# Kernel optimization log

Measured on AMD Instinct MI355X. Metric: run time of the kernel, lower is better.

## Reference

```python
import jax, jax.numpy as jnp
import numpy as np

B, S, D, H = 1, 2048, 768, 12
E, K, I = 8, 2, 1024          # routed experts, top-k, expert inter dim
IS = 2 * I                    # shared-expert inter dim (n_shared_experts * moe_inter_dim)
EPS = 1e-5
ROUTE_SCALE = 1.0


def rmsnorm(x, w, eps=EPS):
    xf = x.astype(jnp.float32)
    return (xf * jax.lax.rsqrt(jnp.mean(xf * xf, axis=-1, keepdims=True) + eps)).astype(x.dtype) * w


def setup_inputs() -> dict:
    key = jax.random.key(0)
    ks = jax.random.split(key, 8)
    sc = 0.02
    return {
        "x": jax.random.normal(ks[0], (B, S, D), jnp.float32),
        "norm1_w": jnp.ones((D,), jnp.float32),
        "norm3_w": jnp.ones((D,), jnp.float32),
        "gate_w": jax.random.normal(ks[1], (E, D), jnp.float32) * sc,
        "w1": jax.random.normal(ks[2], (E, I, D), jnp.float32) * sc,
        "b1": jnp.zeros((E, I), jnp.float32),
        "w2": jax.random.normal(ks[3], (E, D, I), jnp.float32) * sc,
        "b2": jnp.zeros((E, D), jnp.float32),
        "w3": jax.random.normal(ks[4], (E, I, D), jnp.float32) * sc,
        "b3": jnp.zeros((E, I), jnp.float32),
        "fc1_w": jax.random.normal(ks[5], (IS, D), jnp.float32) * sc,
        "fc1_b": jnp.zeros((IS,), jnp.float32),
        "fc2_w": jax.random.normal(ks[6], (D, IS), jnp.float32) * sc,
        "fc2_b": jnp.zeros((D,), jnp.float32),
    }


def _forward(x, norm1_w, norm3_w, gate_w, w1, b1, w2, b2, w3, b3,
             fc1_w, fc1_b, fc2_w, fc2_b):
    b, s, d = x.shape
    hd = d // H

    # ---- self-attention (no qkv/out projections in the original module) ----
    xn = rmsnorm(x, norm1_w)
    qkv = xn.reshape(b, s, H, hd).transpose(0, 2, 1, 3)      # [b,h,s,hd]
    scores = jnp.einsum("bhqd,bhkd->bhqk", qkv, qkv) / np.sqrt(hd)
    attn = jax.nn.softmax(scores, axis=-1)
    ao = jnp.einsum("bhqk,bhkd->bhqd", attn, qkv)
    attn_out = ao.transpose(0, 2, 1, 3).reshape(b, s, d)
    out = x + attn_out

    # ---- MoE on norm3(out) ----
    xf = rmsnorm(out, norm3_w).reshape(-1, d)                # [N, D]
    n = xf.shape[0]

    # Gate: softmax scoring, n_groups=1 (no group masking), no bias (dim != 7168)
    logits = xf @ gate_w.T                                    # [N, E]
    sc = jax.nn.softmax(logits.astype(jnp.float32), axis=-1)  # max-subtract folded in
    _, idx = jax.lax.top_k(sc, K)                             # [N, K]
    weights = jnp.take_along_axis(sc, idx, axis=-1)
    weights = jnp.clip(weights, 1e-7) * ROUTE_SCALE
    weights = weights.astype(xf.dtype)

    # combine matrix: per-token dense expert weights (zeros for unselected)
    cmb = jnp.zeros((n, E), xf.dtype).at[jnp.arange(n)[:, None], idx].add(weights)

    # SwiGLU experts, batched over E (zero combine weight == not dispatched)
    a = jnp.einsum("nd,eid->nei", xf, w1) + b1                # [N,E,I]
    g = jnp.einsum("nd,eid->nei", xf, w3) + b3
    h = jax.nn.silu(a) * g
    eo = jnp.einsum("nei,edi->ned", h, w2) + b2               # [N,E,D]
    y = jnp.einsum("ned,ne->nd", eo, cmb)

    # shared experts (SiLU MLP)
    z = jax.nn.silu(xf @ fc1_w.T + fc1_b) @ fc2_w.T + fc2_b

    moe_out = (y + z).reshape(b, s, d)
    return out + moe_out


def reference(x, norm1_w, norm3_w, gate_w, w1, b1, w2, b2, w3, b3,
              fc1_w, fc1_b, fc2_w, fc2_b):
    return _forward(x, norm1_w, norm3_w, gate_w, w1, b1, w2, b2, w3, b3,
                    fc1_w, fc1_b, fc2_w, fc2_b)
```

## Files before the change

### kernel.cpp

```cpp
#include <hip/hip_runtime.h>
#include <math.h>

#define SEQ    2048
#define DMODEL 768
#define NHEAD  12
#define NEXP   8
#define IDIM   1024
#define ISH    2048
#define KVS    4
#define NE2    10

typedef unsigned short u16;
typedef short s16x8 __attribute__((ext_vector_type(8)));
typedef u16   u16x8 __attribute__((ext_vector_type(8)));
typedef float f32x4 __attribute__((ext_vector_type(4)));

#define MFMA_BF16(a, b, c) __builtin_amdgcn_mfma_f32_16x16x32_bf16((a), (b), (c), 0, 0, 0)

__device__ __forceinline__ void glds16(const void* g, void* l) {
  __builtin_amdgcn_global_load_lds(
      (const __attribute__((address_space(1))) unsigned int*)g,
      (__attribute__((address_space(3))) unsigned int*)l, 16, 0, 0);
}

__device__ __forceinline__ u16 f2b(float f) {
  unsigned int u = __float_as_uint(f);
  unsigned int r = u + 0x7fffu + ((u >> 16) & 1u);
  return (u16)(r >> 16);
}
__device__ __forceinline__ float b2f(u16 v) {
  return __uint_as_float(((unsigned int)v) << 16);
}

__global__ __launch_bounds__(256) void cvt_all_kernel(
    const float* __restrict__ w1, const float* __restrict__ w3, const float* __restrict__ w2,
    const float* __restrict__ fc1, const float* __restrict__ fc2,
    u16* __restrict__ w1b, u16* __restrict__ w3b, u16* __restrict__ w2b,
    u16* __restrict__ fc1b, u16* __restrict__ fc2b, int* __restrict__ counts) {
  if (blockIdx.x == 0 && threadIdx.x < 16) counts[threadIdx.x] = 0;
  long i = (long)blockIdx.x * 256 + threadIdx.x;
  const long NW8 = (long)NEXP * IDIM * DMODEL / 8;
  const long NF8 = (long)ISH * DMODEL / 8;
  const float* s; u16* d; long o;
  if      (i < NW8)             { s = w1;  d = w1b;  o = i; }
  else if (i < 2 * NW8)         { s = w3;  d = w3b;  o = i - NW8; }
  else if (i < 3 * NW8)         { s = w2;  d = w2b;  o = i - 2 * NW8; }
  else if (i < 3 * NW8 + NF8)   { s = fc1; d = fc1b; o = i - 3 * NW8; }
  else if (i < 3 * NW8 + 2*NF8) { s = fc2; d = fc2b; o = i - 3 * NW8 - NF8; }
  else return;
  float4 a = ((const float4*)s)[2 * o], b = ((const float4*)s)[2 * o + 1];
  u16x8 v;
  v[0] = f2b(a.x); v[1] = f2b(a.y); v[2] = f2b(a.z); v[3] = f2b(a.w);
  v[4] = f2b(b.x); v[5] = f2b(b.y); v[6] = f2b(b.z); v[7] = f2b(b.w);
  ((u16x8*)d)[o] = v;
}

__global__ __launch_bounds__(256) void rmsnorm_kernel(const float* __restrict__ in,
                                                      const float* __restrict__ w,
                                                      u16* __restrict__ outb) {
  int row = blockIdx.x;
  int tid = threadIdx.x;
  const float* r = in + (size_t)row * DMODEL;
  float v0 = r[tid], v1 = r[tid + 256], v2 = r[tid + 512];
  float ss = v0 * v0 + v1 * v1 + v2 * v2;
  __shared__ float red[256];
  red[tid] = ss;
  __syncthreads();
  for (int s = 128; s > 0; s >>= 1) {
    if (tid < s) red[tid] += red[tid + s];
    __syncthreads();
  }
  float rms = rsqrtf(red[0] * (1.f / DMODEL) + 1e-5f);
  u16* ob = outb + (size_t)row * DMODEL;
  ob[tid]       = f2b(v0 * rms * w[tid]);
  ob[tid + 256] = f2b(v1 * rms * w[tid + 256]);
  ob[tid + 512] = f2b(v2 * rms * w[tid + 512]);
}

__global__ __launch_bounds__(256) void attn_kernel(const u16* __restrict__ xnb,
                                                   u16* __restrict__ Opart,
                                                   float* __restrict__ Mpart,
                                                   float* __restrict__ Lpart) {
  __shared__ u16 Qs[64][72];
  __shared__ u16 Ks[64][72];
  __shared__ u16 Vt[64][72];
  __shared__ u16 Ps[64][72];
  const int h = blockIdx.y, kvs = blockIdx.z;
  const int q0 = blockIdx.x * 64;
  const int tid = threadIdx.x;
  const int lane = tid & 63, w = tid >> 6;
  const int quad = lane >> 4, l15 = lane & 15;
  const size_t hoff = (size_t)h * 64;

  for (int cc = tid; cc < 512; cc += 256) {
    int row = cc >> 3, col8 = (cc & 7) * 8;
    *(u16x8*)&Qs[row][col8] = *(const u16x8*)(xnb + (size_t)(q0 + row) * DMODEL + hoff + col8);
  }
  __syncthreads();
  const s16x8 aq0 = *(const s16x8*)&Qs[16 * w + l15][quad * 8];
  const s16x8 aq1 = *(const s16x8*)&Qs[16 * w + l15][32 + quad * 8];

  f32x4 o[4] = {};
  float mrow[4], lrow[4];
#pragma unroll
  for (int r = 0; r < 4; r++) { mrow[r] = -INFINITY; lrow[r] = 0.f; }

  const int it0 = kvs * (SEQ / 64 / KVS);
  for (int it = 0; it < SEQ / 64 / KVS; it++) {
    const int k0 = (it0 + it) * 64;
    for (int cc = tid; cc < 512; cc += 256) {
      int row = cc >> 3, col8 = (cc & 7) * 8;
      *(u16x8*)&Ks[row][col8] = *(const u16x8*)(xnb + (size_t)(k0 + row) * DMODEL + hoff + col8);
    }
    __syncthreads();

    {
      const int rp = tid & 31, dc = ((tid >> 5) & 7) * 8;
      u16x8 v0 = *(const u16x8*)&Ks[2 * rp][dc];
      u16x8 v1 = *(const u16x8*)&Ks[2 * rp + 1][dc];
#pragma unroll
      for (int j = 0; j < 8; j++) {
        *(unsigned int*)&Vt[dc + j][2 * rp] =
            (unsigned int)v0[j] | ((unsigned int)v1[j] << 16);
      }
    }

    f32x4 s4[4] = {};
#pragma unroll
    for (int jt = 0; jt < 4; jt++) {
      s16x8 b0 = *(const s16x8*)&Ks[16 * jt + l15][quad * 8];
      s16x8 b1 = *(const s16x8*)&Ks[16 * jt + l15][32 + quad * 8];
      s4[jt] = MFMA_BF16(aq0, b0, s4[jt]);
      s4[jt] = MFMA_BF16(aq1, b1, s4[jt]);
      s4[jt] *= 0.125f;
    }

#pragma unroll
    for (int r = 0; r < 4; r++) {
      float mx = mrow[r];
#pragma unroll
      for (int jt = 0; jt < 4; jt++) mx = fmaxf(mx, s4[jt][r]);
#pragma unroll
      for (int m = 1; m <= 8; m <<= 1) mx = fmaxf(mx, __shfl_xor(mx, m, 64));
      float al = __expf(mrow[r] - mx);
      mrow[r] = mx;
      float pv[4], sum = 0.f;
#pragma unroll
      for (int jt = 0; jt < 4; jt++) { pv[jt] = __expf(s4[jt][r] - mx); sum += pv[jt]; }
#pragma unroll
      for (int m = 1; m <= 8; m <<= 1) sum += __shfl_xor(sum, m, 64);
      lrow[r] = lrow[r] * al + sum;
#pragma unroll
      for (int jt = 0; jt < 4; jt++) o[jt][r] *= al;
#pragma unroll
      for (int jt = 0; jt < 4; jt++) Ps[16 * w + quad * 4 + r][16 * jt + l15] = f2b(pv[jt]);
    }
    __syncthreads();

    s16x8 ap0 = *(const s16x8*)&Ps[16 * w + l15][quad * 8];
    s16x8 ap1 = *(const s16x8*)&Ps[16 * w + l15][32 + quad * 8];
#pragma unroll
    for (int jt = 0; jt < 4; jt++) {
      s16x8 bv0 = *(const s16x8*)&Vt[16 * jt + l15][quad * 8];
      s16x8 bv1 = *(const s16x8*)&Vt[16 * jt + l15][32 + quad * 8];
      o[jt] = MFMA_BF16(ap0, bv0, o[jt]);
      o[jt] = MFMA_BF16(ap1, bv1, o[jt]);
    }
  }

  const size_t base = ((size_t)kvs * NHEAD + h) * SEQ;
#pragma unroll
  for (int r = 0; r < 4; r++) {
    int q = q0 + 16 * w + quad * 4 + r;
#pragma unroll
    for (int jt = 0; jt < 4; jt++)
      Opart[(base + q) * 64 + 16 * jt + l15] = f2b(o[jt][r]);
    if (l15 == 0) {
      Mpart[base + q] = mrow[r];
      Lpart[base + q] = lrow[r];
    }
  }
}

__global__ __launch_bounds__(256) void attn_combine_kernel(const u16* __restrict__ Opart,
                                                           const float* __restrict__ Mpart,
                                                           const float* __restrict__ Lpart,
                                                           const float* __restrict__ x,
                                                           float* __restrict__ outbuf) {
  int idx = blockIdx.x * 256 + threadIdx.x;
  int d = idx & 63, r = idx >> 6;
  int h = r >> 11, q = r & (SEQ - 1);
  float M = -INFINITY;
#pragma unroll
  for (int k = 0; k < KVS; k++) M = fmaxf(M, Mpart[(size_t)k * NHEAD * SEQ + r]);
  float L = 0.f, O = 0.f;
#pragma unroll
  for (int k = 0; k < KVS; k++) {
    size_t pr = (size_t)k * NHEAD * SEQ + r;
    float wgt = __expf(Mpart[pr] - M);
    L += wgt * Lpart[pr];
    O += wgt * b2f(Opart[pr * 64 + d]);
  }
  size_t off = (size_t)q * DMODEL + h * 64 + d;
  outbuf[off] = x[off] + O / L;
}

__global__ __launch_bounds__(256) void gate_kernel(const float* __restrict__ outbuf,
                                                   const float* __restrict__ n3w,
                                                   const float* __restrict__ gw,
                                                   int* __restrict__ topki,
                                                   float* __restrict__ topkw) {
  int lane = threadIdx.x & 63;
  int t = (blockIdx.x * 256 + threadIdx.x) >> 6;
  if (t >= SEQ) return;
  float acc[NEXP] = {};
  float ss = 0.f;
  const float* xr = outbuf + (size_t)t * DMODEL;
  for (int j = 0; j < DMODEL / 64; j++) {
    int d = lane + j * 64;
    float v = xr[d];
    ss += v * v;
    float xn = v * n3w[d];
#pragma unroll
    for (int e = 0; e < NEXP; e++) acc[e] = fmaf(xn, gw[e * DMODEL + d], acc[e]);
  }
#pragma unroll
  for (int off = 32; off >= 1; off >>= 1) {
    ss += __shfl_xor(ss, off, 64);
#pragma unroll
    for (int e = 0; e < NEXP; e++) acc[e] += __shfl_xor(acc[e], off, 64);
  }
  if (lane == 0) {
    float rms = rsqrtf(ss * (1.f / DMODEL) + 1e-5f);
    float mx = -INFINITY;
#pragma unroll
    for (int e = 0; e < NEXP; e++) { acc[e] *= rms; mx = fmaxf(mx, acc[e]); }
    float s = 0.f, p[NEXP];
#pragma unroll
    for (int e = 0; e < NEXP; e++) { p[e] = __expf(acc[e] - mx); s += p[e]; }
    int e0 = 0; float b0 = p[0];
    for (int e = 1; e < NEXP; e++) if (p[e] > b0) { b0 = p[e]; e0 = e; }
    int e1 = -1; float b1v = -1.f;
    for (int e = 0; e < NEXP; e++) if (e != e0 && p[e] > b1v) { b1v = p[e]; e1 = e; }
    float inv = 1.f / s;
    topki[t * 2 + 0] = e0;
    topki[t * 2 + 1] = e1;
    topkw[t * 2 + 0] = fmaxf(b0 * inv, 1e-7f);
    topkw[t * 2 + 1] = fmaxf(b1v * inv, 1e-7f);
  }
}

__global__ void scatter_kernel(const int* __restrict__ topki, const float* __restrict__ topkw,
                               int* __restrict__ counts, int* __restrict__ toklist,
                               float* __restrict__ wtlist) {
  int t = blockIdx.x * blockDim.x + threadIdx.x;
  if (t >= SEQ) return;
#pragma unroll
  for (int k = 0; k < 2; k++) {
    int e = topki[t * 2 + k];
    float w = topkw[t * 2 + k];
    int pos = atomicAdd(&counts[e], 1);
    toklist[e * SEQ + pos] = t;
    wtlist[e * SEQ + pos] = w;
  }
}

__global__ void offsets_kernel(const int* __restrict__ counts, int* __restrict__ offsets) {
  if (threadIdx.x == 0) {
    int o = 0;
    for (int e = 0; e < NEXP; e++) { offsets[e] = o; o += counts[e]; }
  }
}

__global__ __launch_bounds__(256) void copyout_kernel(const float* __restrict__ outbuf,
                                                      float* __restrict__ out) {
  int i = blockIdx.x * 256 + threadIdx.x;
  ((float4*)out)[i] = ((const float4*)outbuf)[i];
}

__global__ __launch_bounds__(256) void gemm1_kernel(
    const u16* __restrict__ xfb,
    const u16* __restrict__ w1b, const u16* __restrict__ w3b, const u16* __restrict__ fc1b,
    const float* __restrict__ b1, const float* __restrict__ b3, const float* __restrict__ fc1_b,
    const int* __restrict__ counts, const int* __restrict__ offsets,
    const int* __restrict__ toklist, u16* __restrict__ hb) {
  __shared__ u16 As[128][32];
  __shared__ u16 W1s[128][32];
  __shared__ u16 W3s[128][32];
  __shared__ int rIdx[128];
  const int e = blockIdx.z;
  const bool routed = (e < NEXP);
  const int cnt = routed ? counts[e] : SEQ;
  const int m0 = blockIdx.y * 128;
  if (m0 >= cnt) return;
  const int n0 = blockIdx.x * 128;
  const int tid = threadIdx.x;
  if (tid < 128) {
    int rr = m0 + tid;
    rIdx[tid] = routed ? toklist[e * SEQ + (rr < cnt ? rr : cnt - 1)] : rr;
  }
  __syncthreads();
  const u16* W1 = routed ? w1b + (size_t)e * IDIM * DMODEL
                         : fc1b + (size_t)(e - NEXP) * IDIM * DMODEL;
  const u16* W3 = w3b + (size_t)(routed ? e : 0) * IDIM * DMODEL;

  const int lane = tid & 63, w = tid >> 6;
  const int quad = lane >> 4, l15 = lane & 15;
  const int wy = w >> 1, wx = w & 1;
  const int s0 = 2 * w, s1 = s0 + 1;
  const int rsub = lane >> 2, c8 = (lane & 3) * 8;
  const u16* Ap0 = xfb + (size_t)rIdx[16 * s0 + rsub] * DMODEL + c8;
  const u16* Ap1 = xfb + (size_t)rIdx[16 * s1 + rsub] * DMODEL + c8;
  const u16* W1p0 = W1 + (size_t)(n0 + 16 * s0 + rsub) * DMODEL + c8;
  const u16* W1p1 = W1 + (size_t)(n0 + 16 * s1 + rsub) * DMODEL + c8;
  const u16* W3p0 = W3 + (size_t)(n0 + 16 * s0 + rsub) * DMODEL + c8;
  const u16* W3p1 = W3 + (size_t)(n0 + 16 * s1 + rsub) * DMODEL + c8;

  f32x4 acc1[4][4] = {};
  f32x4 acc3[4][4] = {};
  for (int k0 = 0; k0 < DMODEL; k0 += 32) {
    glds16(Ap0 + k0, &As[16 * s0][0]);
    glds16(Ap1 + k0, &As[16 * s1][0]);
    glds16(W1p0 + k0, &W1s[16 * s0][0]);
    glds16(W1p1 + k0, &W1s[16 * s1][0]);
    if (routed) {
      glds16(W3p0 + k0, &W3s[16 * s0][0]);
      glds16(W3p1 + k0, &W3s[16 * s1][0]);
    }
    __syncthreads();
    s16x8 af[4], w1f[4];
#pragma unroll
    for (int i = 0; i < 4; i++) af[i] = *(const s16x8*)&As[64 * wy + 16 * i + l15][quad * 8];
#pragma unroll
    for (int j = 0; j < 4; j++) w1f[j] = *(const s16x8*)&W1s[64 * wx + 16 * j + l15][quad * 8];
#pragma unroll
    for (int i = 0; i < 4; i++)
#pragma unroll
      for (int j = 0; j < 4; j++)
        acc1[i][j] = MFMA_BF16(af[i], w1f[j], acc1[i][j]);
    if (routed) {
      s16x8 w3f[4];
#pragma unroll
      for (int j = 0; j < 4; j++) w3f[j] = *(const s16x8*)&W3s[64 * wx + 16 * j + l15][quad * 8];
#pragma unroll
      for (int i = 0; i < 4; i++)
#pragma unroll
        for (int j = 0; j < 4; j++)
          acc3[i][j] = MFMA_BF16(af[i], w3f[j], acc3[i][j]);
    }
    __syncthreads();
  }

  const int off = routed ? offsets[e] : (2 * SEQ + (e - NEXP) * SEQ);
#pragma unroll
  for (int j = 0; j < 4; j++) {
    int n = n0 + 64 * wx + 16 * j + l15;
    float b1v = routed ? b1[e * IDIM + n] : fc1_b[(e - NEXP) * IDIM + n];
    float b3v = routed ? b3[e * IDIM + n] : 0.f;
#pragma unroll
    for (int i = 0; i < 4; i++) {
#pragma unroll
      for (int r = 0; r < 4; r++) {
        int rr = m0 + 64 * wy + 16 * i + quad * 4 + r;
        if (rr < cnt) {
          float a = acc1[i][j][r] + b1v;
          float g = routed ? (acc3[i][j][r] + b3v) : 1.f;
          float hv = a / (1.f + __expf(-a)) * g;
          hb[(size_t)(off + rr) * IDIM + n] = f2b(hv);
        }
      }
    }
  }
}

__global__ __launch_bounds__(256) void gemm2_kernel(
    const u16* __restrict__ hb,
    const u16* __restrict__ w2b, const u16* __restrict__ fc2b,
    const float* __restrict__ b2, const float* __restrict__ fc2_b,
    const int* __restrict__ counts, const int* __restrict__ offsets,
    const int* __restrict__ toklist, const float* __restrict__ wtlist,
    float* __restrict__ out) {
  __shared__ u16 As[128][32];
  __shared__ u16 Ws[128][32];
  const int e = blockIdx.z;
  const bool routed = (e < NEXP);
  const int cnt = routed ? counts[e] : SEQ;
  const int m0 = blockIdx.y * 128;
  if (m0 >= cnt) return;
  const int n0 = blockIdx.x * 128;
  const int tid = threadIdx.x;
  const int off = routed ? offsets[e] : (2 * SEQ + (e - NEXP) * SEQ);

  const u16* Wb; int ldw, kof;
  if (routed) { Wb = w2b + (size_t)e * DMODEL * IDIM; ldw = IDIM; kof = 0; }
  else        { Wb = fc2b;                            ldw = ISH;  kof = (e - NEXP) * IDIM; }

  const int lane = tid & 63, w = tid >> 6;
  const int quad = lane >> 4, l15 = lane & 15;
  const int wy = w >> 1, wx = w & 1;
  const int s0 = 2 * w, s1 = s0 + 1;
  const int rsub = lane >> 2, c8 = (lane & 3) * 8;
  int ra0 = m0 + 16 * s0 + rsub; ra0 = off + (ra0 < cnt ? ra0 : cnt - 1);
  int ra1 = m0 + 16 * s1 + rsub; ra1 = off + (ra1 < cnt ? ra1 : cnt - 1);
  const u16* Ap0 = hb + (size_t)ra0 * IDIM + c8;
  const u16* Ap1 = hb + (size_t)ra1 * IDIM + c8;
  const u16* Wp0 = Wb + (size_t)(n0 + 16 * s0 + rsub) * ldw + kof + c8;
  const u16* Wp1 = Wb + (size_t)(n0 + 16 * s1 + rsub) * ldw + kof + c8;

  f32x4 acc[4][4] = {};
  for (int k0 = 0; k0 < IDIM; k0 += 32) {
    glds16(Ap0 + k0, &As[16 * s0][0]);
    glds16(Ap1 + k0, &As[16 * s1][0]);
    glds16(Wp0 + k0, &Ws[16 * s0][0]);
    glds16(Wp1 + k0, &Ws[16 * s1][0]);
    __syncthreads();
    s16x8 af[4], wf[4];
#pragma unroll
    for (int i = 0; i < 4; i++) af[i] = *(const s16x8*)&As[64 * wy + 16 * i + l15][quad * 8];
#pragma unroll
    for (int j = 0; j < 4; j++) wf[j] = *(const s16x8*)&Ws[64 * wx + 16 * j + l15][quad * 8];
#pragma unroll
    for (int i = 0; i < 4; i++)
#pragma unroll
      for (int j = 0; j < 4; j++)
        acc[i][j] = MFMA_BF16(af[i], wf[j], acc[i][j]);
    __syncthreads();
  }

#pragma unroll
  for (int j = 0; j < 4; j++) {
    int n = n0 + 64 * wx + 16 * j + l15;
    float bv = routed ? b2[e * DMODEL + n] : (e == NEXP ? fc2_b[n] : 0.f);
#pragma unroll
    for (int i = 0; i < 4; i++) {
#pragma unroll
      for (int r = 0; r < 4; r++) {
        int rr = m0 + 64 * wy + 16 * i + quad * 4 + r;
        if (rr < cnt) {
          int tok; float wt;
          if (routed) { tok = toklist[e * SEQ + rr]; wt = wtlist[e * SEQ + rr]; }
          else        { tok = rr;                    wt = 1.f; }
          atomicAdd(&out[(size_t)tok * DMODEL + n], wt * (acc[i][j][r] + bv));
        }
      }
    }
  }
}

extern "C" void kernel_launch(void* const* d_in, const int* in_sizes, int n_in,
                              void* d_out, int out_size, void* d_ws, size_t ws_size,
                              hipStream_t stream) {
  const float* x       = (const float*)d_in[0];
  const float* norm1_w = (const float*)d_in[1];
  const float* norm3_w = (const float*)d_in[2];
  const float* gate_w  = (const float*)d_in[3];
  const float* w1      = (const float*)d_in[4];
  const float* b1      = (const float*)d_in[5];
  const float* w2      = (const float*)d_in[6];
  const float* b2      = (const float*)d_in[7];
  const float* w3      = (const float*)d_in[8];
  const float* b3      = (const float*)d_in[9];
  const float* fc1_w   = (const float*)d_in[10];
  const float* fc1_b   = (const float*)d_in[11];
  const float* fc2_w   = (const float*)d_in[12];
  const float* fc2_b   = (const float*)d_in[13];
  float* out = (float*)d_out;

  char* p = (char*)d_ws;
  u16*   xnb    = (u16*)p;   p += (size_t)SEQ * DMODEL * 2;
  float* outbuf = (float*)p; p += (size_t)SEQ * DMODEL * 4;
  u16*   xfb    = (u16*)p;   p += (size_t)SEQ * DMODEL * 2;
  u16*   hb     = (u16*)p;   p += (size_t)4 * SEQ * IDIM * 2;
  u16*   Opart  = (u16*)p;   p += (size_t)KVS * NHEAD * SEQ * 64 * 2;
  float* Mpart  = (float*)p; p += (size_t)KVS * NHEAD * SEQ * 4;
  float* Lpart  = (float*)p; p += (size_t)KVS * NHEAD * SEQ * 4;
  u16*   w1b    = (u16*)p;   p += (size_t)NEXP * IDIM * DMODEL * 2;
  u16*   w3b    = (u16*)p;   p += (size_t)NEXP * IDIM * DMODEL * 2;
  u16*   w2b    = (u16*)p;   p += (size_t)NEXP * DMODEL * IDIM * 2;
  u16*   fc1b   = (u16*)p;   p += (size_t)ISH * DMODEL * 2;
  u16*   fc2b   = (u16*)p;   p += (size_t)DMODEL * ISH * 2;
  float* topkw  = (float*)p; p += (size_t)SEQ * 2 * 4;
  int*   topki  = (int*)p;   p += (size_t)SEQ * 2 * 4;
  int*   counts = (int*)p;   p += 256;
  int*   offsets= (int*)p;   p += 256;
  int*   toklist= (int*)p;   p += (size_t)NEXP * SEQ * 4;
  float* wtlist = (float*)p; p += (size_t)NEXP * SEQ * 4;

  const long NW8 = (long)NEXP * IDIM * DMODEL / 8;
  const long NF8 = (long)ISH * DMODEL / 8;
  const int cvt_blocks = (int)((3 * NW8 + 2 * NF8 + 255) / 256);
  cvt_all_kernel<<<cvt_blocks, 256, 0, stream>>>(w1, w3, w2, fc1_w, fc2_w,
                                                 w1b, w3b, w2b, fc1b, fc2b, counts);
  rmsnorm_kernel<<<SEQ, 256, 0, stream>>>(x, norm1_w, xnb);
  attn_kernel<<<dim3(SEQ / 64, NHEAD, KVS), 256, 0, stream>>>(xnb, Opart, Mpart, Lpart);
  attn_combine_kernel<<<NHEAD * SEQ * 64 / 256, 256, 0, stream>>>(Opart, Mpart, Lpart, x, outbuf);
  rmsnorm_kernel<<<SEQ, 256, 0, stream>>>(outbuf, norm3_w, xfb);
  gate_kernel<<<SEQ * 64 / 256, 256, 0, stream>>>(outbuf, norm3_w, gate_w, topki, topkw);
  scatter_kernel<<<SEQ / 256, 256, 0, stream>>>(topki, topkw, counts, toklist, wtlist);
  offsets_kernel<<<1, 64, 0, stream>>>(counts, offsets);
  gemm1_kernel<<<dim3(IDIM / 128, SEQ / 128, NE2), 256, 0, stream>>>(
      xfb, w1b, w3b, fc1b, b1, b3, fc1_b, counts, offsets, toklist, hb);
  copyout_kernel<<<SEQ * DMODEL / 4 / 256, 256, 0, stream>>>(outbuf, out);
  gemm2_kernel<<<dim3(DMODEL / 128, SEQ / 128, NE2), 256, 0, stream>>>(
      hb, w2b, fc2b, b2, fc2_b, counts, offsets, toklist, wtlist, out);
  (void)in_sizes; (void)n_in; (void)out_size; (void)ws_size;
}
```

Measured before the change: 377.6 us.

## Fuse attention combine, norm, gate and scatter; shrink MoE GEMM M-tile to 64

Merges the attention partial-combine, residual add, RMSNorm, gate softmax/top-k and token scatter into one per-token kernel that writes the residual straight to the output. This removes the outbuf round trip, the copy-out kernel and several small launches. The expert offsets are now computed inside each GEMM block from counts. Both MoE GEMMs also drop their row tile from 128 to 64, which gives more blocks and less wasted padding on the uneven per-expert row counts, at the cost of less weight reuse per block.

New measurement: 352.8 us. 6.6% less time.

```diff
diff --git a/kernel.cpp b/kernel.cpp
--- a/kernel.cpp
+++ b/kernel.cpp
@@ -182,120 +182,118 @@
   }
 }
 
-__global__ __launch_bounds__(256) void attn_combine_kernel(const u16* __restrict__ Opart,
-                                                           const float* __restrict__ Mpart,
-                                                           const float* __restrict__ Lpart,
-                                                           const float* __restrict__ x,
-                                                           float* __restrict__ outbuf) {
-  int idx = blockIdx.x * 256 + threadIdx.x;
-  int d = idx & 63, r = idx >> 6;
-  int h = r >> 11, q = r & (SEQ - 1);
-  float M = -INFINITY;
-#pragma unroll
-  for (int k = 0; k < KVS; k++) M = fmaxf(M, Mpart[(size_t)k * NHEAD * SEQ + r]);
-  float L = 0.f, O = 0.f;
-#pragma unroll
-  for (int k = 0; k < KVS; k++) {
-    size_t pr = (size_t)k * NHEAD * SEQ + r;
-    float wgt = __expf(Mpart[pr] - M);
-    L += wgt * Lpart[pr];
-    O += wgt * b2f(Opart[pr * 64 + d]);
-  }
-  size_t off = (size_t)q * DMODEL + h * 64 + d;
-  outbuf[off] = x[off] + O / L;
-}
-
-__global__ __launch_bounds__(256) void gate_kernel(const float* __restrict__ outbuf,
-                                                   const float* __restrict__ n3w,
-                                                   const float* __restrict__ gw,
-                                                   int* __restrict__ topki,
-                                                   float* __restrict__ topkw) {
-  int lane = threadIdx.x & 63;
-  int t = (blockIdx.x * 256 + threadIdx.x) >> 6;
-  if (t >= SEQ) return;
-  float acc[NEXP] = {};
+__global__ __launch_bounds__(256) void fused_post_kernel(
+    const u16* __restrict__ Opart, const float* __restrict__ Mpart,
+    const float* __restrict__ Lpart, const float* __restrict__ x,
+    const float* __restrict__ n3w, const float* __restrict__ gw,
+    u16* __restrict__ xfb, float* __restrict__ out,
+    int* __restrict__ counts, int* __restrict__ toklist, float* __restrict__ wtlist) {
+  const int t = blockIdx.x;
+  const int tid = threadIdx.x;
+  __shared__ float Ms[KVS * NHEAD], Ls[KVS * NHEAD];
+  __shared__ float red[256];
+  __shared__ float gred[4][NEXP];
+  if (tid < KVS * NHEAD) {
+    Ms[tid] = Mpart[(size_t)tid * SEQ + t];
+    Ls[tid] = Lpart[(size_t)tid * SEQ + t];
+  }
+  __syncthreads();
+
+  float val[3];
   float ss = 0.f;
-  const float* xr = outbuf + (size_t)t * DMODEL;
-  for (int j = 0; j < DMODEL / 64; j++) {
-    int d = lane + j * 64;
-    float v = xr[d];
+#pragma unroll
+  for (int ii = 0; ii < 3; ii++) {
+    int c = tid + ii * 256;
+    int h = c >> 6, d = c & 63;
+    float M = -INFINITY;
+#pragma unroll
+    for (int k = 0; k < KVS; k++) M = fmaxf(M, Ms[k * NHEAD + h]);
+    float L = 0.f, O = 0.f;
+#pragma unroll
+    for (int k = 0; k < KVS; k++) {
+      float wgt = __expf(Ms[k * NHEAD + h] - M);
+      L += wgt * Ls[k * NHEAD + h];
+      O += wgt * b2f(Opart[((size_t)(k * NHEAD + h) * SEQ + t) * 64 + d]);
+    }
+    float v = x[(size_t)t * DMODEL + c] + O / L;
+    out[(size_t)t * DMODEL + c] = v;
+    val[ii] = v;
     ss += v * v;
-    float xn = v * n3w[d];
-#pragma unroll
-    for (int e = 0; e < NEXP; e++) acc[e] = fmaf(xn, gw[e * DMODEL + d], acc[e]);
-  }
-#pragma unroll
-  for (int off = 32; off >= 1; off >>= 1) {
-    ss += __shfl_xor(ss, off, 64);
-#pragma unroll
-    for (int e = 0; e < NEXP; e++) acc[e] += __shfl_xor(acc[e], off, 64);
-  }
-  if (lane == 0) {
-    float rms = rsqrtf(ss * (1.f / DMODEL) + 1e-5f);
-    float mx = -INFINITY;
-#pragma unroll
-    for (int e = 0; e < NEXP; e++) { acc[e] *= rms; mx = fmaxf(mx, acc[e]); }
-    float s = 0.f, p[NEXP];
-#pragma unroll
-    for (int e = 0; e < NEXP; e++) { p[e] = __expf(acc[e] - mx); s += p[e]; }
+  }
+  red[tid] = ss;
+  __syncthreads();
+  for (int s = 128; s > 0; s >>= 1) {
+    if (tid < s) red[tid] += red[tid + s];
+    __syncthreads();
+  }
+  float rms = rsqrtf(red[0] * (1.f / DMODEL) + 1e-5f);
+
+  float ge[NEXP] = {};
+#pragma unroll
+  for (int ii = 0; ii < 3; ii++) {
+    int c = tid + ii * 256;
+    float xn = val[ii] * rms * n3w[c];
+    xfb[(size_t)t * DMODEL + c] = f2b(xn);
+#pragma unroll
+    for (int e = 0; e < NEXP; e++) ge[e] = fmaf(xn, gw[e * DMODEL + c], ge[e]);
+  }
+  const int lane = tid & 63, w = tid >> 6;
+#pragma unroll
+  for (int off = 32; off >= 1; off >>= 1)
+#pragma unroll
+    for (int e = 0; e < NEXP; e++) ge[e] += __shfl_xor(ge[e], off, 64);
+  if (lane == 0)
+#pragma unroll
+    for (int e = 0; e < NEXP; e++) gred[w][e] = ge[e];
+  __syncthreads();
+  if (tid == 0) {
+    float p[NEXP], mx = -INFINITY, s = 0.f;
+#pragma unroll
+    for (int e = 0; e < NEXP; e++) {
+      p[e] = gred[0][e] + gred[1][e] + gred[2][e] + gred[3][e];
+      mx = fmaxf(mx, p[e]);
+    }
+#pragma unroll
+    for (int e = 0; e < NEXP; e++) { p[e] = __expf(p[e] - mx); s += p[e]; }
     int e0 = 0; float b0 = p[0];
     for (int e = 1; e < NEXP; e++) if (p[e] > b0) { b0 = p[e]; e0 = e; }
     int e1 = -1; float b1v = -1.f;
     for (int e = 0; e < NEXP; e++) if (e != e0 && p[e] > b1v) { b1v = p[e]; e1 = e; }
     float inv = 1.f / s;
-    topki[t * 2 + 0] = e0;
-    topki[t * 2 + 1] = e1;
-    topkw[t * 2 + 0] = fmaxf(b0 * inv, 1e-7f);
-    topkw[t * 2 + 1] = fmaxf(b1v * inv, 1e-7f);
-  }
-}
-
-__global__ void scatter_kernel(const int* __restrict__ topki, const float* __restrict__ topkw,
-                               int* __restrict__ counts, int* __restrict__ toklist,
-                               float* __restrict__ wtlist) {
-  int t = blockIdx.x * blockDim.x + threadIdx.x;
-  if (t >= SEQ) return;
-#pragma unroll
-  for (int k = 0; k < 2; k++) {
-    int e = topki[t * 2 + k];
-    float w = topkw[t * 2 + k];
-    int pos = atomicAdd(&counts[e], 1);
-    toklist[e * SEQ + pos] = t;
-    wtlist[e * SEQ + pos] = w;
-  }
-}
-
-__global__ void offsets_kernel(const int* __restrict__ counts, int* __restrict__ offsets) {
-  if (threadIdx.x == 0) {
-    int o = 0;
-    for (int e = 0; e < NEXP; e++) { offsets[e] = o; o += counts[e]; }
-  }
-}
-
-__global__ __launch_bounds__(256) void copyout_kernel(const float* __restrict__ outbuf,
-                                                      float* __restrict__ out) {
-  int i = blockIdx.x * 256 + threadIdx.x;
-  ((float4*)out)[i] = ((const float4*)outbuf)[i];
+    int pos0 = atomicAdd(&counts[e0], 1);
+    toklist[e0 * SEQ + pos0] = t;
+    wtlist[e0 * SEQ + pos0] = fmaxf(b0 * inv, 1e-7f);
+    int pos1 = atomicAdd(&counts[e1], 1);
+    toklist[e1 * SEQ + pos1] = t;
+    wtlist[e1 * SEQ + pos1] = fmaxf(b1v * inv, 1e-7f);
+  }
 }
 
 __global__ __launch_bounds__(256) void gemm1_kernel(
     const u16* __restrict__ xfb,
     const u16* __restrict__ w1b, const u16* __restrict__ w3b, const u16* __restrict__ fc1b,
     const float* __restrict__ b1, const float* __restrict__ b3, const float* __restrict__ fc1_b,
-    const int* __restrict__ counts, const int* __restrict__ offsets,
-    const int* __restrict__ toklist, u16* __restrict__ hb) {
-  __shared__ u16 As[128][32];
+    const int* __restrict__ counts, const int* __restrict__ toklist, u16* __restrict__ hb) {
+  __shared__ u16 As[64][32];
   __shared__ u16 W1s[128][32];
   __shared__ u16 W3s[128][32];
-  __shared__ int rIdx[128];
+  __shared__ int rIdx[64];
   const int e = blockIdx.z;
   const bool routed = (e < NEXP);
-  const int cnt = routed ? counts[e] : SEQ;
-  const int m0 = blockIdx.y * 128;
+  int cnt, off;
+  if (routed) {
+    cnt = counts[e];
+    off = 0;
+    for (int i = 0; i < e; i++) off += counts[i];
+  } else {
+    cnt = SEQ;
+    off = 2 * SEQ + (e - NEXP) * SEQ;
+  }
+  const int m0 = blockIdx.y * 64;
   if (m0 >= cnt) return;
   const int n0 = blockIdx.x * 128;
   const int tid = threadIdx.x;
-  if (tid < 128) {
+  if (tid < 64) {
     int rr = m0 + tid;
     rIdx[tid] = routed ? toklist[e * SEQ + (rr < cnt ? rr : cnt - 1)] : rr;
   }
@@ -307,34 +305,31 @@
   const int lane = tid & 63, w = tid >> 6;
   const int quad = lane >> 4, l15 = lane & 15;
   const int wy = w >> 1, wx = w & 1;
-  const int s0 = 2 * w, s1 = s0 + 1;
   const int rsub = lane >> 2, c8 = (lane & 3) * 8;
-  const u16* Ap0 = xfb + (size_t)rIdx[16 * s0 + rsub] * DMODEL + c8;
-  const u16* Ap1 = xfb + (size_t)rIdx[16 * s1 + rsub] * DMODEL + c8;
-  const u16* W1p0 = W1 + (size_t)(n0 + 16 * s0 + rsub) * DMODEL + c8;
-  const u16* W1p1 = W1 + (size_t)(n0 + 16 * s1 + rsub) * DMODEL + c8;
-  const u16* W3p0 = W3 + (size_t)(n0 + 16 * s0 + rsub) * DMODEL + c8;
-  const u16* W3p1 = W3 + (size_t)(n0 + 16 * s1 + rsub) * DMODEL + c8;
-
-  f32x4 acc1[4][4] = {};
-  f32x4 acc3[4][4] = {};
+  const u16* Ap   = xfb + (size_t)rIdx[16 * w + rsub] * DMODEL + c8;
+  const u16* W1p0 = W1 + (size_t)(n0 + 32 * w + rsub) * DMODEL + c8;
+  const u16* W1p1 = W1 + (size_t)(n0 + 32 * w + 16 + rsub) * DMODEL + c8;
+  const u16* W3p0 = W3 + (size_t)(n0 + 32 * w + rsub) * DMODEL + c8;
+  const u16* W3p1 = W3 + (size_t)(n0 + 32 * w + 16 + rsub) * DMODEL + c8;
+
+  f32x4 acc1[2][4] = {};
+  f32x4 acc3[2][4] = {};
   for (int k0 = 0; k0 < DMODEL; k0 += 32) {
-    glds16(Ap0 + k0, &As[16 * s0][0]);
-    glds16(Ap1 + k0, &As[16 * s1][0]);
-    glds16(W1p0 + k0, &W1s[16 * s0][0]);
-    glds16(W1p1 + k0, &W1s[16 * s1][0]);
+    glds16(Ap + k0, &As[16 * w][0]);
+    glds16(W1p0 + k0, &W1s[32 * w][0]);
+    glds16(W1p1 + k0, &W1s[32 * w + 16][0]);
     if (routed) {
-      glds16(W3p0 + k0, &W3s[16 * s0][0]);
-      glds16(W3p1 + k0, &W3s[16 * s1][0]);
-    }
-    __syncthreads();
-    s16x8 af[4], w1f[4];
-#pragma unroll
-    for (int i = 0; i < 4; i++) af[i] = *(const s16x8*)&As[64 * wy + 16 * i + l15][quad * 8];
+      glds16(W3p0 + k0, &W3s[32 * w][0]);
+      glds16(W3p1 + k0, &W3s[32 * w + 16][0]);
+    }
+    __syncthreads();
+    s16x8 af[2], w1f[4];
+#pragma unroll
+    for (int i = 0; i < 2; i++) af[i] = *(const s16x8*)&As[32 * wy + 16 * i + l15][quad * 8];
 #pragma unroll
     for (int j = 0; j < 4; j++) w1f[j] = *(const s16x8*)&W1s[64 * wx + 16 * j + l15][quad * 8];
 #pragma unroll
-    for (int i = 0; i < 4; i++)
+    for (int i = 0; i < 2; i++)
 #pragma unroll
       for (int j = 0; j < 4; j++)
         acc1[i][j] = MFMA_BF16(af[i], w1f[j], acc1[i][j]);
@@ -343,7 +338,7 @@
 #pragma unroll
       for (int j = 0; j < 4; j++) w3f[j] = *(const s16x8*)&W3s[64 * wx + 16 * j + l15][quad * 8];
 #pragma unroll
-      for (int i = 0; i < 4; i++)
+      for (int i = 0; i < 2; i++)
 #pragma unroll
         for (int j = 0; j < 4; j++)
           acc3[i][j] = MFMA_BF16(af[i], w3f[j], acc3[i][j]);
@@ -351,17 +346,16 @@
     __syncthreads();
   }
 
-  const int off = routed ? offsets[e] : (2 * SEQ + (e - NEXP) * SEQ);
 #pragma unroll
   for (int j = 0; j < 4; j++) {
     int n = n0 + 64 * wx + 16 * j + l15;
     float b1v = routed ? b1[e * IDIM + n] : fc1_b[(e - NEXP) * IDIM + n];
     float b3v = routed ? b3[e * IDIM + n] : 0.f;
 #pragma unroll
-    for (int i = 0; i < 4; i++) {
+    for (int i = 0; i < 2; i++) {
 #pragma unroll
       for (int r = 0; r < 4; r++) {
-        int rr = m0 + 64 * wy + 16 * i + quad * 4 + r;
+        int rr = m0 + 32 * wy + 16 * i + quad * 4 + r;
         if (rr < cnt) {
           float a = acc1[i][j][r] + b1v;
           float g = routed ? (acc3[i][j][r] + b3v) : 1.f;
@@ -377,19 +371,25 @@
     const u16* __restrict__ hb,
     const u16* __restrict__ w2b, const u16* __restrict__ fc2b,
     const float* __restrict__ b2, const float* __restrict__ fc2_b,
-    const int* __restrict__ counts, const int* __restrict__ offsets,
-    const int* __restrict__ toklist, const float* __restrict__ wtlist,
-    float* __restrict__ out) {
-  __shared__ u16 As[128][32];
+    const int* __restrict__ counts, const int* __restrict__ toklist,
+    const float* __restrict__ wtlist, float* __restrict__ out) {
+  __shared__ u16 As[64][32];
   __shared__ u16 Ws[128][32];
   const int e = blockIdx.z;
   const bool routed = (e < NEXP);
-  const int cnt = routed ? counts[e] : SEQ;
-  const int m0 = blockIdx.y * 128;
+  int cnt, off;
+  if (routed) {
+    cnt = counts[e];
+    off = 0;
+    for (int i = 0; i < e; i++) off += counts[i];
+  } else {
+    cnt = SEQ;
+    off = 2 * SEQ + (e - NEXP) * SEQ;
+  }
+  const int m0 = blockIdx.y * 64;
   if (m0 >= cnt) return;
   const int n0 = blockIdx.x * 128;
   const int tid = threadIdx.x;
-  const int off = routed ? offsets[e] : (2 * SEQ + (e - NEXP) * SEQ);
 
   const u16* Wb; int ldw, kof;
   if (routed) { Wb = w2b + (size_t)e * DMODEL * IDIM; ldw = IDIM; kof = 0; }
@@ -398,29 +398,25 @@
   const int lane = tid & 63, w = tid >> 6;
   const int quad = lane >> 4, l15 = lane & 15;
   const int wy = w >> 1, wx = w & 1;
-  const int s0 = 2 * w, s1 = s0 + 1;
   const int rsub = lane >> 2, c8 = (lane & 3) * 8;
-  int ra0 = m0 + 16 * s0 + rsub; ra0 = off + (ra0 < cnt ? ra0 : cnt - 1);
-  int ra1 = m0 + 16 * s1 + rsub; ra1 = off + (ra1 < cnt ? ra1 : cnt - 1);
-  const u16* Ap0 = hb + (size_t)ra0 * IDIM + c8;
-  const u16* Ap1 = hb + (size_t)ra1 * IDIM + c8;
-  const u16* Wp0 = Wb + (size_t)(n0 + 16 * s0 + rsub) * ldw + kof + c8;
-  const u16* Wp1 = Wb + (size_t)(n0 + 16 * s1 + rsub) * ldw + kof + c8;
-
-  f32x4 acc[4][4] = {};
+  int ra = m0 + 16 * w + rsub; ra = off + (ra < cnt ? ra : cnt - 1);
+  const u16* Ap  = hb + (size_t)ra * IDIM + c8;
+  const u16* Wp0 = Wb + (size_t)(n0 + 32 * w + rsub) * ldw + kof + c8;
+  const u16* Wp1 = Wb + (size_t)(n0 + 32 * w + 16 + rsub) * ldw + kof + c8;
+
+  f32x4 acc[2][4] = {};
   for (int k0 = 0; k0 < IDIM; k0 += 32) {
-    glds16(Ap0 + k0, &As[16 * s0][0]);
-    glds16(Ap1 + k0, &As[16 * s1][0]);
-    glds16(Wp0 + k0, &Ws[16 * s0][0]);
-    glds16(Wp1 + k0, &Ws[16 * s1][0]);
-    __syncthreads();
-    s16x8 af[4], wf[4];
-#pragma unroll
-    for (int i = 0; i < 4; i++) af[i] = *(const s16x8*)&As[64 * wy + 16 * i + l15][quad * 8];
+    glds16(Ap + k0, &As[16 * w][0]);
+    glds16(Wp0 + k0, &Ws[32 * w][0]);
+    glds16(Wp1 + k0, &Ws[32 * w + 16][0]);
+    __syncthreads();
+    s16x8 af[2], wf[4];
+#pragma unroll
+    for (int i = 0; i < 2; i++) af[i] = *(const s16x8*)&As[32 * wy + 16 * i + l15][quad * 8];
 #pragma unroll
     for (int j = 0; j < 4; j++) wf[j] = *(const s16x8*)&Ws[64 * wx + 16 * j + l15][quad * 8];
 #pragma unroll
-    for (int i = 0; i < 4; i++)
+    for (int i = 0; i < 2; i++)
 #pragma unroll
       for (int j = 0; j < 4; j++)
         acc[i][j] = MFMA_BF16(af[i], wf[j], acc[i][j]);
@@ -432,10 +428,10 @@
     int n = n0 + 64 * wx + 16 * j + l15;
     float bv = routed ? b2[e * DMODEL + n] : (e == NEXP ? fc2_b[n] : 0.f);
 #pragma unroll
-    for (int i = 0; i < 4; i++) {
+    for (int i = 0; i < 2; i++) {
 #pragma unroll
       for (int r = 0; r < 4; r++) {
-        int rr = m0 + 64 * wy + 16 * i + quad * 4 + r;
+        int rr = m0 + 32 * wy + 16 * i + quad * 4 + r;
         if (rr < cnt) {
           int tok; float wt;
           if (routed) { tok = toklist[e * SEQ + rr]; wt = wtlist[e * SEQ + rr]; }
@@ -468,7 +464,6 @@
 
   char* p = (char*)d_ws;
   u16*   xnb    = (u16*)p;   p += (size_t)SEQ * DMODEL * 2;
-  float* outbuf = (float*)p; p += (size_t)SEQ * DMODEL * 4;
   u16*   xfb    = (u16*)p;   p += (size_t)SEQ * DMODEL * 2;
   u16*   hb     = (u16*)p;   p += (size_t)4 * SEQ * IDIM * 2;
   u16*   Opart  = (u16*)p;   p += (size_t)KVS * NHEAD * SEQ * 64 * 2;
@@ -479,10 +474,7 @@
   u16*   w2b    = (u16*)p;   p += (size_t)NEXP * DMODEL * IDIM * 2;
   u16*   fc1b   = (u16*)p;   p += (size_t)ISH * DMODEL * 2;
   u16*   fc2b   = (u16*)p;   p += (size_t)DMODEL * ISH * 2;
-  float* topkw  = (float*)p; p += (size_t)SEQ * 2 * 4;
-  int*   topki  = (int*)p;   p += (size_t)SEQ * 2 * 4;
   int*   counts = (int*)p;   p += 256;
-  int*   offsets= (int*)p;   p += 256;
   int*   toklist= (int*)p;   p += (size_t)NEXP * SEQ * 4;
   float* wtlist = (float*)p; p += (size_t)NEXP * SEQ * 4;
 
@@ -493,15 +485,11 @@
                                                  w1b, w3b, w2b, fc1b, fc2b, counts);
   rmsnorm_kernel<<<SEQ, 256, 0, stream>>>(x, norm1_w, xnb);
   attn_kernel<<<dim3(SEQ / 64, NHEAD, KVS), 256, 0, stream>>>(xnb, Opart, Mpart, Lpart);
-  attn_combine_kernel<<<NHEAD * SEQ * 64 / 256, 256, 0, stream>>>(Opart, Mpart, Lpart, x, outbuf);
-  rmsnorm_kernel<<<SEQ, 256, 0, stream>>>(outbuf, norm3_w, xfb);
-  gate_kernel<<<SEQ * 64 / 256, 256, 0, stream>>>(outbuf, norm3_w, gate_w, topki, topkw);
-  scatter_kernel<<<SEQ / 256, 256, 0, stream>>>(topki, topkw, counts, toklist, wtlist);
-  offsets_kernel<<<1, 64, 0, stream>>>(counts, offsets);
-  gemm1_kernel<<<dim3(IDIM / 128, SEQ / 128, NE2), 256, 0, stream>>>(
-      xfb, w1b, w3b, fc1b, b1, b3, fc1_b, counts, offsets, toklist, hb);
-  copyout_kernel<<<SEQ * DMODEL / 4 / 256, 256, 0, stream>>>(outbuf, out);
-  gemm2_kernel<<<dim3(DMODEL / 128, SEQ / 128, NE2), 256, 0, stream>>>(
-      hb, w2b, fc2b, b2, fc2_b, counts, offsets, toklist, wtlist, out);
+  fused_post_kernel<<<SEQ, 256, 0, stream>>>(Opart, Mpart, Lpart, x, norm3_w, gate_w,
+                                             xfb, out, counts, toklist, wtlist);
+  gemm1_kernel<<<dim3(IDIM / 128, SEQ / 64, NE2), 256, 0, stream>>>(
+      xfb, w1b, w3b, fc1b, b1, b3, fc1_b, counts, toklist, hb);
+  gemm2_kernel<<<dim3(DMODEL / 128, SEQ / 64, NE2), 256, 0, stream>>>(
+      hb, w2b, fc2b, b2, fc2_b, counts, toklist, wtlist, out);
   (void)in_sizes; (void)n_in; (void)out_size; (void)ws_size;
 }
```
